# Kernel optimization log

Hardware: AMD Instinct MI355X
Metric: run time of the kernel (lower is better)

Reference implementation:

```python
import jax, jax.numpy as jnp
import numpy as np

N_STEPS = 5
N_ETYPES = 4
N_GRAPHS = 64
HEADS = 2
N, E, D = 50000, 600000, 128
C = 32


def setup_inputs() -> dict:
    key = jax.random.key(0)
    ks = jax.random.split(key, 24)
    s = 0.08  # param scale to keep activations well-conditioned
    return {
        "in_feat1": jax.random.normal(ks[0], (N, D), jnp.float32),
        "in_feat2": jax.random.normal(ks[1], (N, D), jnp.float32),
        "src1": jax.random.randint(ks[2], (E,), 0, N, jnp.int32),
        "dst1": jax.random.randint(ks[3], (E,), 0, N, jnp.int32),
        "etype1": jax.random.randint(ks[4], (E,), 0, N_ETYPES, jnp.int32),
        "gid1": jnp.sort(jax.random.randint(ks[5], (N,), 0, N_GRAPHS, jnp.int32)),
        "src2": jax.random.randint(ks[6], (E,), 0, N, jnp.int32),
        "dst2": jax.random.randint(ks[7], (E,), 0, N, jnp.int32),
        "etype2": jax.random.randint(ks[8], (E,), 0, N_ETYPES, jnp.int32),
        "gid2": jnp.sort(jax.random.randint(ks[9], (N,), 0, N_GRAPHS, jnp.int32)),
        "W_et": jax.random.normal(ks[10], (N_ETYPES, D, D), jnp.float32) * s,
        "b_et": jax.random.normal(ks[11], (N_ETYPES, D), jnp.float32) * s,
        "W_ih": jax.random.normal(ks[12], (3 * D, D), jnp.float32) * s,
        "W_hh": jax.random.normal(ks[13], (3 * D, D), jnp.float32) * s,
        "b_ih": jax.random.normal(ks[14], (3 * D,), jnp.float32) * s,
        "b_hh": jax.random.normal(ks[15], (3 * D,), jnp.float32) * s,
        "W_fc": jax.random.normal(ks[16], (HEADS * D, D), jnp.float32) * s,
        "attn_l": jax.random.normal(ks[17], (HEADS, D), jnp.float32) * s,
        "attn_r": jax.random.normal(ks[18], (HEADS, D), jnp.float32) * s,
        "gat_bias": jax.random.normal(ks[19], (HEADS * D,), jnp.float32) * s,
        "W_cls": jax.random.normal(ks[20], (C, D), jnp.float32) * s,
        "b_cls": jax.random.normal(ks[21], (C,), jnp.float32) * s,
    }


def _ggann(feat, src, dst, etype, gid,
           W_et, b_et, W_ih, W_hh, b_ih, b_hh,
           W_fc, attn_l, attn_r, gat_bias, W_cls, b_cls):
    n = feat.shape[0]
    h = feat  # in_feats == out_feats -> no zero-padding needed
    # ---- GatedGraphConv: n_steps of per-etype message passing + GRU ----
    for _ in range(N_STEPS):
        # per-etype linear on all nodes: [K, N, D]
        t = jnp.einsum('kod,nd->kno', W_et, h) + b_et[:, None, :]
        msg = t[etype, src]                         # [E, D] gather by (etype, src)
        a = jax.ops.segment_sum(msg, dst, num_segments=n)  # [N, D]
        # GRUCell(a, h)
        gi = a @ W_ih.T + b_ih                      # [N, 3D]
        gh = h @ W_hh.T + b_hh
        i_r, i_z, i_n = jnp.split(gi, 3, axis=1)
        h_r, h_z, h_n = jnp.split(gh, 3, axis=1)
        r = jax.nn.sigmoid(i_r + h_r)
        z = jax.nn.sigmoid(i_z + h_z)
        nn_ = jnp.tanh(i_n + r * h_n)
        h = (1.0 - z) * nn_ + z * h
    # F.normalize (L2 over dim=1) then sigmoid
    h = h / jnp.maximum(jnp.linalg.norm(h, axis=1, keepdims=True), 1e-12)
    h = jax.nn.sigmoid(h)
    # ---- GATConv (num_heads=2) ----
    zft = (h @ W_fc.T).reshape(n, HEADS, D)         # [N, H, D]
    el = jnp.sum(zft * attn_l[None], axis=-1)       # [N, H]
    er = jnp.sum(zft * attn_r[None], axis=-1)
    e = jax.nn.leaky_relu(el[src] + er[dst], 0.2)   # [E, H]
    m = jax.ops.segment_max(e, dst, num_segments=n)
    ex = jnp.exp(e - m[dst])
    den = jax.ops.segment_sum(ex, dst, num_segments=n)
    alpha = ex / den[dst]                           # edge softmax per dst, per head
    rst = jax.ops.segment_sum(alpha[:, :, None] * zft[src], dst, num_segments=n)
    rst = rst + gat_bias.reshape(1, HEADS, D)
    h = jax.nn.relu(rst)                            # [N, H, D] (dropout = eval identity)
    # ---- mean_nodes per graph + classify ----
    sums = jax.ops.segment_sum(h, gid, num_segments=N_GRAPHS)      # [B, H, D]
    cnt = jax.ops.segment_sum(jnp.ones((n, 1, 1), h.dtype), gid, num_segments=N_GRAPHS)
    hg = sums / jnp.maximum(cnt, 1.0)
    return hg @ W_cls.T + b_cls                     # [B, H, C]


def reference(in_feat1, in_feat2, src1, dst1, etype1, gid1,
              src2, dst2, etype2, gid2,
              W_et, b_et, W_ih, W_hh, b_ih, b_hh,
              W_fc, attn_l, attn_r, gat_bias, W_cls, b_cls):
    params = (W_et, b_et, W_ih, W_hh, b_ih, b_hh,
              W_fc, attn_l, attn_r, gat_bias, W_cls, b_cls)
    h1 = _ggann(in_feat1, src1, dst1, etype1, gid1, *params)  # [B, H, C]
    h2 = _ggann(in_feat2, src2, dst2, etype2, gid2, *params)
    # F.pairwise_distance(p=2, eps=1e-6) over last dim -> [B, H]
    dist = jnp.linalg.norm(h1 - h2 + 1e-6, axis=-1)
    return jax.nn.softmax(dist, axis=1)             # softmax over the 2 heads
```

## Files before the change

### kernel.cpp

```cpp
#include <hip/hip_runtime.h>
#include <math.h>

#define D 128
#define NG 64
#define NG2 128
#define NSTEPS 5

using short8 = __attribute__((ext_vector_type(8))) short;
using f32x4  = __attribute__((ext_vector_type(4))) float;
using f32x2  = __attribute__((ext_vector_type(2))) float;

__device__ __forceinline__ float sigf(float x) {
  float e = __expf(-fabsf(x));
  float inv = __fdividef(1.f, 1.f + e);
  return x >= 0.f ? inv : e * inv;
}
__device__ __forceinline__ float tanhf_fast(float x) {
  float e = __expf(-2.f * fabsf(x));
  float r = (1.f - e) * __fdividef(1.f, 1.f + e);
  return x >= 0.f ? r : -r;
}
__device__ __forceinline__ float lrelu(float x) { return x > 0.f ? x : 0.2f * x; }
__device__ __forceinline__ short f2bf(float x) {
  unsigned u = __float_as_uint(x);
  u += 0x7fff + ((u >> 16) & 1);
  return (short)(u >> 16);
}
__device__ __forceinline__ unsigned pk2(float x, float y) {
  return ((unsigned)(unsigned short)f2bf(y) << 16) | (unsigned short)f2bf(x);
}
__device__ __forceinline__ float bflo(unsigned v) { return __uint_as_float(v << 16); }
__device__ __forceinline__ float bfhi(unsigned v) { return __uint_as_float(v & 0xffff0000u); }
__device__ __forceinline__ float bf2f(short s) {
  return __uint_as_float(((unsigned)(unsigned short)s) << 16);
}
__device__ __forceinline__ unsigned char f2fp8(float x) {
  int p = __builtin_amdgcn_cvt_pk_fp8_f32(x, x, 0, false);
  return (unsigned char)(p & 0xff);
}

__device__ __forceinline__ void packK128(const float* __restrict__ W,
                                         short* __restrict__ P, int i) {
  int j = i & 7;
  int lane = (i >> 3) & 63;
  int kt = (i >> 9) & 3;
  int nt = i >> 11;
  int c = nt * 16 + (lane & 15);
  int k = kt * 32 + ((lane >> 4) << 3) + j;
  P[i] = f2bf(W[c * 128 + k]);
}
__device__ __forceinline__ void packA512f(const float* __restrict__ W_et,
                                          short* __restrict__ P, int i) {
  int j = i & 7;
  int lane = (i >> 3) & 63;
  int kt = (i >> 9) & 15;
  int nt = i >> 13;
  int c = nt * 16 + (lane & 15);
  int k = kt * 32 + ((lane >> 4) << 3) + j;
  P[i] = f2bf(W_et[(k >> 7) * 16384 + c * 128 + (k & 127)]);
}

__global__ __launch_bounds__(256) void k_setup(const float* __restrict__ W_et,
    const float* __restrict__ W_ih, const float* __restrict__ W_hh,
    const float* __restrict__ W_fc, const float* __restrict__ f1,
    const float* __restrict__ f2, short* __restrict__ WaP, short* __restrict__ WihP,
    short* __restrict__ WhhP, short* __restrict__ WfcP, short* __restrict__ hb,
    unsigned char* __restrict__ hq,
    int* __restrict__ deg, int* __restrict__ gcnt, int N2, int Nd4) {
  const int sA = 65536, sB = 49152, sC = 49152, sD = 32768;
  int sE = N2, sF = NG2;
  long sG = 2L * Nd4;
  long tot = (long)(sA + sB + sC + sD) + sE + sF + sG;
  for (long ii = (long)blockIdx.x * blockDim.x + threadIdx.x; ii < tot;
       ii += (long)gridDim.x * blockDim.x) {
    long r = ii;
    if (r < sA) { packA512f(W_et, WaP, (int)r); continue; }
    r -= sA;
    if (r < sB) { packK128(W_ih, WihP, (int)r); continue; }
    r -= sB;
    if (r < sC) { packK128(W_hh, WhhP, (int)r); continue; }
    r -= sC;
    if (r < sD) { packK128(W_fc, WfcP, (int)r); continue; }
    r -= sD;
    if (r < sE) { deg[r] = 0; continue; }
    r -= sE;
    if (r < sF) { gcnt[r] = 0; continue; }
    r -= sF;
    {
      int i = (int)r;
      float4 v = (i < Nd4) ? ((const float4*)f1)[i] : ((const float4*)f2)[i - Nd4];
      ((uint2*)hb)[i] = make_uint2(pk2(v.x, v.y), pk2(v.z, v.w));
      int q = __builtin_amdgcn_cvt_pk_fp8_f32(v.x, v.y, 0, false);
      q = __builtin_amdgcn_cvt_pk_fp8_f32(v.z, v.w, q, true);
      ((unsigned*)hq)[i] = (unsigned)q;
    }
  }
}

__global__ __launch_bounds__(256) void k_histgid(const int* __restrict__ dst1,
    const int* __restrict__ dst2, const int* __restrict__ gid1,
    const int* __restrict__ gid2, int E, int N, int* __restrict__ deg,
    int* __restrict__ gidc, int* __restrict__ gcnt, int EB, int N2) {
  __shared__ int cnt[NG2];
  if ((int)blockIdx.x < EB) {
    int slice = blockIdx.x & 7;
    int bls = blockIdx.x >> 3;
    int nbs = EB >> 3;
    int W = (N2 + 7) >> 3;
    int lo = slice * W, hi = lo + W;
    for (int e = bls * 256 + threadIdx.x; e < 2 * E; e += nbs * 256) {
      int d = (e < E) ? dst1[e] : dst2[e - E] + N;
      if (d >= lo && d < hi) atomicAdd(&deg[d], 1);
    }
  } else {
    int t = threadIdx.x;
    if (t < NG2) cnt[t] = 0;
    __syncthreads();
    int i = (blockIdx.x - EB) * 256 + t;
    if (i < 2 * N) {
      int g = (i < N) ? gid1[i] : gid2[i - N] + NG;
      gidc[i] = g;
      atomicAdd(&cnt[g], 1);
    }
    __syncthreads();
    if (t < NG2 && cnt[t]) atomicAdd(&gcnt[t], cnt[t]);
  }
}

__global__ __launch_bounds__(256) void k_scan_a(const int* __restrict__ deg, int n,
                                                int* __restrict__ bsum) {
  int base = blockIdx.x * 1024 + threadIdx.x * 4;
  int s = 0;
  if (base + 3 < n) {
    int4 v = *(const int4*)(deg + base);
    s = v.x + v.y + v.z + v.w;
  } else {
    for (int k = 0; k < 4; ++k) if (base + k < n) s += deg[base + k];
  }
  #pragma unroll
  for (int off = 32; off; off >>= 1) s += __shfl_xor(s, off);
  __shared__ int ws[4];
  if ((threadIdx.x & 63) == 0) ws[threadIdx.x >> 6] = s;
  __syncthreads();
  if (threadIdx.x == 0) bsum[blockIdx.x] = ws[0] + ws[1] + ws[2] + ws[3];
}

__global__ __launch_bounds__(1024) void k_scan_b(const int* __restrict__ bsum,
                                                 int* __restrict__ boffs, int nb) {
  int tid = threadIdx.x;
  int v = (tid < nb) ? bsum[tid] : 0;
  int lane = tid & 63, wv = tid >> 6;
  int x = v;
  #pragma unroll
  for (int off = 1; off < 64; off <<= 1) {
    int y = __shfl_up(x, off);
    if (lane >= off) x += y;
  }
  __shared__ int wsum[16];
  if (lane == 63) wsum[wv] = x;
  __syncthreads();
  if (tid < 16) {
    int u = wsum[tid];
    #pragma unroll
    for (int off = 1; off < 16; off <<= 1) {
      int y = __shfl_up(u, off);
      if (tid >= off) u += y;
    }
    wsum[tid] = u;
  }
  __syncthreads();
  int woff = wv ? wsum[wv - 1] : 0;
  if (tid < nb) boffs[tid] = woff + x - v;
}

__global__ __launch_bounds__(256) void k_scan_c(const int* __restrict__ deg,
    const int* __restrict__ boffs, int* __restrict__ row_ofs,
    int* __restrict__ cursor, int n) {
  int base = blockIdx.x * 1024 + threadIdx.x * 4;
  int v[4] = {0, 0, 0, 0};
  if (base + 3 < n) {
    int4 t = *(const int4*)(deg + base);
    v[0] = t.x; v[1] = t.y; v[2] = t.z; v[3] = t.w;
  } else {
    for (int k = 0; k < 4; ++k) if (base + k < n) v[k] = deg[base + k];
  }
  int s = v[0] + v[1] + v[2] + v[3];
  int lane = threadIdx.x & 63, wv = threadIdx.x >> 6;
  int x = s;
  #pragma unroll
  for (int off = 1; off < 64; off <<= 1) {
    int y = __shfl_up(x, off);
    if (lane >= off) x += y;
  }
  __shared__ int wsum[4];
  if (lane == 63) wsum[wv] = x;
  __syncthreads();
  int woff = 0;
  for (int w = 0; w < wv; ++w) woff += wsum[w];
  int run = boffs[blockIdx.x] + woff + x - s;
  #pragma unroll
  for (int k = 0; k < 4; ++k) {
    int i = base + k;
    if (i < n) {
      cursor[i] = run;
      run += v[k];
      row_ofs[i + 1] = run;
    }
  }
  if (blockIdx.x == 0 && threadIdx.x == 0) row_ofs[0] = 0;
}

__global__ __launch_bounds__(256) void k_scatter(const int* __restrict__ src1,
    const int* __restrict__ dst1, const int* __restrict__ ety1,
    const int* __restrict__ src2, const int* __restrict__ dst2,
    const int* __restrict__ ety2, int E, int N, int* __restrict__ cursor,
    int* __restrict__ csr_se, int N2) {
  int slice = blockIdx.x & 7;
  int bls = blockIdx.x >> 3;
  int nbs = gridDim.x >> 3;
  int W = (N2 + 7) >> 3;
  int lo = slice * W, hi = lo + W;
  for (int e = bls * 256 + threadIdx.x; e < 2 * E; e += nbs * 256) {
    int d = (e < E) ? dst1[e] : dst2[e - E] + N;
    if (d < lo || d >= hi) continue;
    int s, et;
    if (e < E) { s = src1[e]; et = ety1[e]; }
    else { s = src2[e - E] + N; et = ety2[e - E]; }
    int p = atomicAdd(&cursor[d], 1);
    csr_se[p] = (s << 10) + et;
  }
}

__global__ __launch_bounds__(1024) void k_step(const unsigned char* __restrict__ hq_old,
    const short* __restrict__ hb_old, unsigned char* __restrict__ hq_new,
    short* __restrict__ hb_new,
    const int* __restrict__ row_ofs, const int* __restrict__ csr_se,
    const short* __restrict__ WaP, const float* __restrict__ b_et,
    const short* __restrict__ Pih, const short* __restrict__ Phh,
    const float* __restrict__ b_ih, const float* __restrict__ b_hh, int M) {
  __shared__ short Stile[16 * 512];
  __shared__ float lcnt[16][4];
  __shared__ short abt[16 * 128];
  __shared__ short hin[16 * 128];
  __shared__ short hbs[16 * 128];
  __shared__ unsigned char hqs[16 * 128];
  int tid = threadIdx.x;
  int lane = tid & 63, wave = tid >> 6;
  int row0 = blockIdx.x * 16;
  int quad = lane >> 4, l15 = lane & 15;

  {
    int li = wave;
    int node = row0 + li;
    f32x2 A0 = {0.f, 0.f}, A1 = {0.f, 0.f}, A2 = {0.f, 0.f}, A3 = {0.f, 0.f};
    int c0 = 0, c1 = 0, c2 = 0, c3 = 0;
    const char* hqb = (const char*)hq_old;
    if (node < M) {
      int beg = row_ofs[node], end = row_ofs[node + 1];
      #define ACC(ET, V) do { \
          f32x2 t_ = __builtin_amdgcn_cvt_pk_f32_fp8((unsigned)(V), false); \
          if (ET == 0)      { A0 += t_; ++c0; } \
          else if (ET == 1) { A1 += t_; ++c1; } \
          else if (ET == 2) { A2 += t_; ++c2; } \
          else              { A3 += t_; ++c3; } } while (0)
      for (int base = beg; base < end; base += 64) {
        int nv = end - base; if (nv > 64) nv = 64;
        int r = (lane < nv) ? csr_se[base + lane] : 0;
        int j = 0;
        for (; j + 16 <= nv; j += 16) {
          int rr[16];
          #pragma unroll
          for (int k = 0; k < 16; ++k) rr[k] = __builtin_amdgcn_readlane(r, j + k);
          unsigned short v[16];
          #pragma unroll
          for (int k = 0; k < 16; ++k)
            v[k] = ((const unsigned short*)(hqb + (rr[k] >> 3)))[lane];
          #pragma unroll
          for (int k = 0; k < 16; ++k) ACC(rr[k] & 3, v[k]);
        }
        for (; j + 8 <= nv; j += 8) {
          int rr[8];
          #pragma unroll
          for (int k = 0; k < 8; ++k) rr[k] = __builtin_amdgcn_readlane(r, j + k);
          unsigned short v[8];
          #pragma unroll
          for (int k = 0; k < 8; ++k)
            v[k] = ((const unsigned short*)(hqb + (rr[k] >> 3)))[lane];
          #pragma unroll
          for (int k = 0; k < 8; ++k) ACC(rr[k] & 3, v[k]);
        }
        for (; j + 4 <= nv; j += 4) {
          int rr[4];
          #pragma unroll
          for (int k = 0; k < 4; ++k) rr[k] = __builtin_amdgcn_readlane(r, j + k);
          unsigned short v[4];
          #pragma unroll
          for (int k = 0; k < 4; ++k)
            v[k] = ((const unsigned short*)(hqb + (rr[k] >> 3)))[lane];
          #pragma unroll
          for (int k = 0; k < 4; ++k) ACC(rr[k] & 3, v[k]);
        }
        for (; j < nv; ++j) {
          int rr = __builtin_amdgcn_readlane(r, j);
          unsigned short v = ((const unsigned short*)(hqb + (rr >> 3)))[lane];
          ACC(rr & 3, v);
        }
      }
      #undef ACC
    }
    int swz = (li & 7) << 4;
    unsigned* ld = (unsigned*)Stile;
    ld[(li * 1024 + ((lane * 4      ) ^ swz)) >> 2] = pk2(A0[0], A0[1]);
    ld[(li * 1024 + ((lane * 4 + 256) ^ swz)) >> 2] = pk2(A1[0], A1[1]);
    ld[(li * 1024 + ((lane * 4 + 512) ^ swz)) >> 2] = pk2(A2[0], A2[1]);
    ld[(li * 1024 + ((lane * 4 + 768) ^ swz)) >> 2] = pk2(A3[0], A3[1]);
    if (lane == 0) {
      lcnt[li][0] = (float)c0; lcnt[li][1] = (float)c1;
      lcnt[li][2] = (float)c2; lcnt[li][3] = (float)c3;
    }
  }
  __syncthreads();

  if (wave < 8) {
    int swz = (l15 & 7) << 4;
    int nt = wave;
    f32x4 acc = {0.f, 0.f, 0.f, 0.f};
    #pragma unroll
    for (int kt = 0; kt < 16; ++kt) {
      int boff = l15 * 1024 + ((kt * 64 + quad * 16) ^ swz);
      short8 a = *(const short8*)((const char*)Stile + boff);
      short8 b = *(const short8*)(WaP + (((size_t)(nt * 16 + kt) * 64) + lane) * 8);
      acc = __builtin_amdgcn_mfma_f32_16x16x32_bf16(a, b, acc, 0, 0, 0);
    }
    int c = nt * 16 + l15;
    float be0 = b_et[c], be1 = b_et[128 + c], be2 = b_et[256 + c], be3 = b_et[384 + c];
    #pragma unroll
    for (int reg = 0; reg < 4; ++reg) {
      int lr = quad * 4 + reg;
      float v = acc[reg] + lcnt[lr][0] * be0 + lcnt[lr][1] * be1
                         + lcnt[lr][2] * be2 + lcnt[lr][3] * be3;
      int bo = (lr * 256 + c * 2) ^ ((lr & 7) << 4);
      *(short*)((char*)abt + bo) = f2bf(v);
    }
  } else if (wave < 12) {
    int t2 = tid - 512;
    int row = t2 >> 4;
    int col8 = t2 & 15;
    int r = row0 + row;
    uint4 v = make_uint4(0, 0, 0, 0);
    if (r < M) v = *(const uint4*)(hb_old + (size_t)r * 128 + col8 * 8);
    int bo = (row * 256 + col8 * 16) ^ ((row & 7) << 4);
    *(uint4*)((char*)hin + bo) = v;
  }
  __syncthreads();

  if (wave < 8) {
    int nt = wave;
    size_t li = ((size_t)lane) * 8;
    f32x4 accr = {0.f,0.f,0.f,0.f}, accz = {0.f,0.f,0.f,0.f};
    f32x4 acci = {0.f,0.f,0.f,0.f}, acch = {0.f,0.f,0.f,0.f};
    #pragma unroll
    for (int kt = 0; kt < 4; ++kt) {
      int ao = (l15 * 256 + (kt * 64 + quad * 16)) ^ ((l15 & 7) << 4);
      short8 fa = *(const short8*)((const char*)abt + ao);
      short8 fh = *(const short8*)((const char*)hin + ao);
      short8 wr = *(const short8*)(Pih + ((size_t)((nt     ) * 4 + kt) * 64) * 8 + li);
      short8 wz = *(const short8*)(Pih + ((size_t)((nt +  8) * 4 + kt) * 64) * 8 + li);
      short8 wn = *(const short8*)(Pih + ((size_t)((nt + 16) * 4 + kt) * 64) * 8 + li);
      short8 ur = *(const short8*)(Phh + ((size_t)((nt     ) * 4 + kt) * 64) * 8 + li);
      short8 uz = *(const short8*)(Phh + ((size_t)((nt +  8) * 4 + kt) * 64) * 8 + li);
      short8 un = *(const short8*)(Phh + ((size_t)((nt + 16) * 4 + kt) * 64) * 8 + li);
      accr = __builtin_amdgcn_mfma_f32_16x16x32_bf16(fa, wr, accr, 0, 0, 0);
      accr = __builtin_amdgcn_mfma_f32_16x16x32_bf16(fh, ur, accr, 0, 0, 0);
      accz = __builtin_amdgcn_mfma_f32_16x16x32_bf16(fa, wz, accz, 0, 0, 0);
      accz = __builtin_amdgcn_mfma_f32_16x16x32_bf16(fh, uz, accz, 0, 0, 0);
      acci = __builtin_amdgcn_mfma_f32_16x16x32_bf16(fa, wn, acci, 0, 0, 0);
      acch = __builtin_amdgcn_mfma_f32_16x16x32_bf16(fh, un, acch, 0, 0, 0);
    }
    int c = nt * 16 + l15;
    float bir = b_ih[c],      bhr = b_hh[c];
    float biz = b_ih[c+128],  bhz = b_hh[c+128];
    float bin_= b_ih[c+256],  bhn = b_hh[c+256];
    #pragma unroll
    for (int reg = 0; reg < 4; ++reg) {
      int lr = quad * 4 + reg;
      float rgate = sigf(accr[reg] + bir + bhr);
      float zg = sigf(accz[reg] + biz + bhz);
      float ng = tanhf_fast(acci[reg] + bin_ + rgate * (acch[reg] + bhn));
      int ho = (lr * 256 + c * 2) ^ ((lr & 7) << 4);
      float hold = bf2f(*(const short*)((const char*)hin + ho));
      float hn2 = (1.f - zg) * ng + zg * hold;
      hbs[lr * 128 + c] = f2bf(hn2);
      hqs[lr * 128 + c] = f2fp8(hn2);
    }
  }
  __syncthreads();

  if (tid < 256) {
    int off16 = tid * 8;
    int grow = off16 >> 7;
    if (row0 + grow < M)
      *(uint4*)(hb_new + (size_t)row0 * 128 + off16) = *(const uint4*)&hbs[off16];
  } else if (tid < 384) {
    int offb = (tid - 256) * 16;
    int grow = offb >> 7;
    if (row0 + grow < M)
      *(uint4*)(hq_new + (size_t)row0 * 128 + offb) = *(const uint4*)&hqs[offb];
  }
}

__global__ __launch_bounds__(256) void k_fc_eler(const short* __restrict__ Ab,
    const short* __restrict__ Bp, const float* __restrict__ attn_l,
    const float* __restrict__ attn_r, unsigned char* __restrict__ zq,
    float* __restrict__ el, float* __restrict__ er, int M) {
  int tid = threadIdx.x;
  int lane = tid & 63, wave = tid >> 6;
  int row0 = blockIdx.x * 128 + wave * 32;
  int quad = lane >> 4, l15 = lane & 15;
  short8 af[2][4];
  #pragma unroll
  for (int rt = 0; rt < 2; ++rt) {
    int ar = row0 + rt * 16 + l15; if (ar >= M) ar = M - 1;
    #pragma unroll
    for (int kt = 0; kt < 4; ++kt)
      af[rt][kt] = *(const short8*)(Ab + (size_t)ar * 128 + kt * 32 + quad * 8);
  }
  #pragma unroll
  for (int rt = 0; rt < 2; ++rt) {
    float ss = 0.f;
    #pragma unroll
    for (int kt = 0; kt < 4; ++kt)
      #pragma unroll
      for (int j = 0; j < 8; ++j) {
        float x = bf2f(af[rt][kt][j]);
        ss += x * x;
      }
    ss += __shfl_xor(ss, 16);
    ss += __shfl_xor(ss, 32);
    float inv = 1.f / fmaxf(sqrtf(ss), 1e-12f);
    #pragma unroll
    for (int kt = 0; kt < 4; ++kt)
      #pragma unroll
      for (int j = 0; j < 8; ++j)
        af[rt][kt][j] = f2bf(sigf(bf2f(af[rt][kt][j]) * inv));
  }
  float elp[2][2][4] = {};
  float erp[2][2][4] = {};
  for (int nt = 0; nt < 16; ++nt) {
    f32x4 a0 = {0.f,0.f,0.f,0.f}, a1 = {0.f,0.f,0.f,0.f};
    #pragma unroll
    for (int kt = 0; kt < 4; ++kt) {
      short8 b = *(const short8*)(Bp + (((size_t)(nt * 4 + kt) * 64) + lane) * 8);
      a0 = __builtin_amdgcn_mfma_f32_16x16x32_bf16(af[0][kt], b, a0, 0, 0, 0);
      a1 = __builtin_amdgcn_mfma_f32_16x16x32_bf16(af[1][kt], b, a1, 0, 0, 0);
    }
    int head = nt >> 3;
    int colh = (nt & 7) * 16 + l15;
    float alv = attn_l[head * 128 + colh];
    float arv = attn_r[head * 128 + colh];
    int c = nt * 16 + l15;
    #pragma unroll
    for (int rt = 0; rt < 2; ++rt) {
      f32x4 acc = rt ? a1 : a0;
      #pragma unroll
      for (int reg = 0; reg < 4; ++reg) {
        int r = row0 + rt * 16 + quad * 4 + reg;
        if (r < M) zq[(size_t)r * 256 + c] = f2fp8(acc[reg]);
        elp[rt][head][reg] += acc[reg] * alv;
        erp[rt][head][reg] += acc[reg] * arv;
      }
    }
  }
  #pragma unroll
  for (int off = 1; off < 16; off <<= 1) {
    #pragma unroll
    for (int rt = 0; rt < 2; ++rt)
      #pragma unroll
      for (int h = 0; h < 2; ++h)
        #pragma unroll
        for (int reg = 0; reg < 4; ++reg) {
          elp[rt][h][reg] += __shfl_xor(elp[rt][h][reg], off);
          erp[rt][h][reg] += __shfl_xor(erp[rt][h][reg], off);
        }
  }
  if (l15 == 0) {
    #pragma unroll
    for (int rt = 0; rt < 2; ++rt)
      #pragma unroll
      for (int h = 0; h < 2; ++h)
        #pragma unroll
        for (int reg = 0; reg < 4; ++reg) {
          int r = row0 + rt * 16 + quad * 4 + reg;
          if (r < M) {
            el[r * 2 + h] = elp[rt][h][reg];
            er[r * 2 + h] = erp[rt][h][reg];
          }
        }
  }
}

__global__ __launch_bounds__(256) void k_gat(const unsigned char* __restrict__ zq,
    const float* __restrict__ el, const float* __restrict__ er,
    const int* __restrict__ row_ofs, const int* __restrict__ csr_se,
    const float* __restrict__ gat_bias, short* __restrict__ outb,
    float* __restrict__ sums, int N) {
  if (blockIdx.x < NG2) sums[blockIdx.x * 256 + threadIdx.x] = 0.f;
  int node = blockIdx.x * 4 + (threadIdx.x >> 6);
  int lane = threadIdx.x & 63;
  if (node >= N) return;
  int beg = row_ofs[node], end = row_ofs[node + 1];
  float2 ern = ((const float2*)er)[node];
  float l0 = 0.f, l1 = 0.f;
  float4 acc = {0.f, 0.f, 0.f, 0.f};
  int head = lane >> 5;
  const char* elb = (const char*)el;
  const char* zqb = (const char*)zq;
  for (int base = beg; base < end; base += 64) {
    int nv = end - base; if (nv > 64) nv = 64;
    int se = (lane < nv) ? csr_se[base + lane] : 0;
    float p0 = 0.f, p1 = 0.f;
    if (lane < nv) {
      float2 els = *(const float2*)(elb + (se >> 7));
      p0 = expf(lrelu(els.x + ern.x));
      p1 = expf(lrelu(els.y + ern.y));
    }
    float t0 = p0, t1 = p1;
    #pragma unroll
    for (int off = 32; off; off >>= 1) { t0 += __shfl_xor(t0, off); t1 += __shfl_xor(t1, off); }
    l0 += t0; l1 += t1;
    int w01 = (int)pk2(p0, p1);
    int j = 0;
    for (; j + 8 <= nv; j += 8) {
      int bb[8]; unsigned ww[8];
      #pragma unroll
      for (int k = 0; k < 8; ++k) {
        bb[k] = __builtin_amdgcn_readlane(se, j + k) >> 2;
        ww[k] = (unsigned)__builtin_amdgcn_readlane(w01, j + k);
      }
      unsigned zz[8];
      #pragma unroll
      for (int k = 0; k < 8; ++k)
        zz[k] = ((const unsigned*)(zqb + bb[k]))[lane];
      #pragma unroll
      for (int k = 0; k < 8; ++k) {
        float f = head ? bfhi(ww[k]) : bflo(ww[k]);
        f32x2 lo = __builtin_amdgcn_cvt_pk_f32_fp8(zz[k], false);
        f32x2 hi = __builtin_amdgcn_cvt_pk_f32_fp8(zz[k], true);
        acc.x += f * lo[0]; acc.y += f * lo[1];
        acc.z += f * hi[0]; acc.w += f * hi[1];
      }
    }
    for (; j + 4 <= nv; j += 4) {
      int bb[4]; unsigned ww[4];
      #pragma unroll
      for (int k = 0; k < 4; ++k) {
        bb[k] = __builtin_amdgcn_readlane(se, j + k) >> 2;
        ww[k] = (unsigned)__builtin_amdgcn_readlane(w01, j + k);
      }
      unsigned zz[4];
      #pragma unroll
      for (int k = 0; k < 4; ++k)
        zz[k] = ((const unsigned*)(zqb + bb[k]))[lane];
      #pragma unroll
      for (int k = 0; k < 4; ++k) {
        float f = head ? bfhi(ww[k]) : bflo(ww[k]);
        f32x2 lo = __builtin_amdgcn_cvt_pk_f32_fp8(zz[k], false);
        f32x2 hi = __builtin_amdgcn_cvt_pk_f32_fp8(zz[k], true);
        acc.x += f * lo[0]; acc.y += f * lo[1];
        acc.z += f * hi[0]; acc.w += f * hi[1];
      }
    }
    for (; j < nv; ++j) {
      int bj = __builtin_amdgcn_readlane(se, j) >> 2;
      unsigned wj = (unsigned)__builtin_amdgcn_readlane(w01, j);
      float w = head ? bfhi(wj) : bflo(wj);
      unsigned zv = ((const unsigned*)(zqb + bj))[lane];
      f32x2 lo = __builtin_amdgcn_cvt_pk_f32_fp8(zv, false);
      f32x2 hi = __builtin_amdgcn_cvt_pk_f32_fp8(zv, true);
      acc.x += w * lo[0]; acc.y += w * lo[1];
      acc.z += w * hi[0]; acc.w += w * hi[1];
    }
  }
  float inv0 = (l0 > 0.f) ? 1.f / l0 : 0.f;
  float inv1 = (l1 > 0.f) ? 1.f / l1 : 0.f;
  float inv = head ? inv1 : inv0;
  float4 b = ((const float4*)gat_bias)[lane];
  float ox = fmaxf(acc.x * inv + b.x, 0.f);
  float oy = fmaxf(acc.y * inv + b.y, 0.f);
  float oz = fmaxf(acc.z * inv + b.z, 0.f);
  float ow = fmaxf(acc.w * inv + b.w, 0.f);
  ((uint2*)(outb + (size_t)node * 256))[lane] = make_uint2(pk2(ox, oy), pk2(oz, ow));
}

__global__ __launch_bounds__(256) void k_segred(const short* __restrict__ hgatb,
    const int* __restrict__ gidc, float* __restrict__ sums, int NT2) {
  int node0 = blockIdx.x * 128;
  int col = threadIdx.x;
  int end = node0 + 128; if (end > NT2) end = NT2;
  if (node0 >= NT2) return;
  float acc = 0.f;
  int gcur = gidc[node0];
  for (int n = node0; n < end; ++n) {
    int g = gidc[n];
    if (g != gcur) {
      atomicAdd(&sums[gcur * 256 + col], acc);
      acc = 0.f; gcur = g;
    }
    acc += bf2f(hgatb[(size_t)n * 256 + col]);
  }
  atomicAdd(&sums[gcur * 256 + col], acc);
}

__global__ __launch_bounds__(64) void k_classify(const float* __restrict__ sums,
    const int* __restrict__ gcnt, const float* __restrict__ W_cls,
    const float* __restrict__ b_cls, float* __restrict__ logits) {
  int g = blockIdx.x, tid = threadIdx.x;
  int hh = tid >> 5, c = tid & 31;
  float invc = 1.f / fmaxf((float)gcnt[g], 1.f);
  float acc = 0.f;
  for (int d = 0; d < D; ++d)
    acc += (sums[g * 256 + hh * D + d] * invc) * W_cls[c * D + d];
  logits[g * 64 + hh * 32 + c] = acc + b_cls[c];
}

__global__ __launch_bounds__(64) void k_final(const float* __restrict__ logits,
    float* __restrict__ out) {
  int g = threadIdx.x;
  if (g >= NG) return;
  float d[2];
  #pragma unroll
  for (int hh = 0; hh < 2; ++hh) {
    float s = 0.f;
    for (int c = 0; c < 32; ++c) {
      float df = logits[g * 64 + hh * 32 + c] - logits[(g + NG) * 64 + hh * 32 + c] + 1e-6f;
      s += df * df;
    }
    d[hh] = sqrtf(s);
  }
  float mx = fmaxf(d[0], d[1]);
  float e0 = expf(d[0] - mx), e1 = expf(d[1] - mx);
  float den = e0 + e1;
  out[g * 2] = e0 / den;
  out[g * 2 + 1] = e1 / den;
}

extern "C" void kernel_launch(void* const* d_in, const int* in_sizes, int n_in,
                              void* d_out, int out_size, void* d_ws, size_t ws_size,
                              hipStream_t stream) {
  const float* in_feat1 = (const float*)d_in[0];
  const float* in_feat2 = (const float*)d_in[1];
  const int* src1 = (const int*)d_in[2];
  const int* dst1 = (const int*)d_in[3];
  const int* ety1 = (const int*)d_in[4];
  const int* gid1 = (const int*)d_in[5];
  const int* src2 = (const int*)d_in[6];
  const int* dst2 = (const int*)d_in[7];
  const int* ety2 = (const int*)d_in[8];
  const int* gid2 = (const int*)d_in[9];
  const float* W_et = (const float*)d_in[10];
  const float* b_et = (const float*)d_in[11];
  const float* W_ih = (const float*)d_in[12];
  const float* W_hh = (const float*)d_in[13];
  const float* b_ih = (const float*)d_in[14];
  const float* b_hh = (const float*)d_in[15];
  const float* W_fc = (const float*)d_in[16];
  const float* attn_l = (const float*)d_in[17];
  const float* attn_r = (const float*)d_in[18];
  const float* gat_bias = (const float*)d_in[19];
  const float* W_cls = (const float*)d_in[20];
  const float* b_cls = (const float*)d_in[21];
  float* out = (float*)d_out;

  int N = in_sizes[0] / D;
  int E = in_sizes[2];
  int N2 = 2 * N, E2 = 2 * E;

  char* p = (char*)d_ws;
  auto alloc = [&](size_t bytes) -> void* {
    char* r = p;
    p += (bytes + 255) & ~(size_t)255;
    return (void*)r;
  };
  short* WaP  = (short*)alloc((size_t)512 * 128 * 2);
  short* WihP = (short*)alloc((size_t)384 * 128 * 2);
  short* WhhP = (short*)alloc((size_t)384 * 128 * 2);
  short* WfcP = (short*)alloc((size_t)256 * 128 * 2);
  short* hb0 = (short*)alloc((size_t)N2 * D * 2);
  short* hb1 = (short*)alloc((size_t)N2 * D * 2);
  unsigned char* hq0 = (unsigned char*)alloc((size_t)N2 * D);
  unsigned char* hq1 = (unsigned char*)alloc((size_t)N2 * D);
  short* hgatb = (short*)alloc((size_t)N2 * 256 * 2);
  unsigned char* zq = (unsigned char*)alloc((size_t)N2 * 256);
  float* el  = (float*)alloc((size_t)N2 * 2 * 4);
  float* er  = (float*)alloc((size_t)N2 * 2 * 4);
  float* sums= (float*)alloc((size_t)NG2 * 256 * 4);
  float* logits = (float*)alloc((size_t)NG2 * 64 * 4);
  int* deg     = (int*)alloc((size_t)N2 * 4);
  int* row_ofs = (int*)alloc(((size_t)N2 + 1) * 4);
  int* cursor  = (int*)alloc((size_t)N2 * 4);
  int* gidc    = (int*)alloc((size_t)N2 * 4);
  int* gcnt    = (int*)alloc((size_t)NG2 * 4);
  int* bsum    = (int*)alloc((size_t)1024 * 4);
  int* boffs   = (int*)alloc((size_t)1024 * 4);
  int* csr_se  = (int*)alloc((size_t)E2 * 4);
  if ((size_t)(p - (char*)d_ws) > ws_size) return;

  k_setup<<<dim3(2048), dim3(256), 0, stream>>>(W_et, W_ih, W_hh, W_fc,
      in_feat1, in_feat2, WaP, WihP, WhhP, WfcP, hb0, hq0, deg, gcnt, N2, N * D / 4);

  int EB = 4800;
  int GB = (N2 + 255) / 256;
  int nb = (N2 + 1023) / 1024;
  k_histgid<<<dim3(EB + GB), dim3(256), 0, stream>>>(dst1, dst2, gid1, gid2,
                                                     E, N, deg, gidc, gcnt, EB, N2);
  k_scan_a<<<dim3(nb), dim3(256), 0, stream>>>(deg, N2, bsum);
  k_scan_b<<<dim3(1), dim3(1024), 0, stream>>>(bsum, boffs, nb);
  k_scan_c<<<dim3(nb), dim3(256), 0, stream>>>(deg, boffs, row_ofs, cursor, N2);
  k_scatter<<<dim3(4800), dim3(256), 0, stream>>>(src1, dst1, ety1, src2, dst2, ety2,
                                                  E, N, cursor, csr_se, N2);

  int gb16 = (N2 + 15) / 16;
  int gb128 = (N2 + 127) / 128;
  int nb4 = (N2 + 3) / 4;

  short* hbp[2] = {hb0, hb1};
  unsigned char* hqp[2] = {hq0, hq1};
  for (int s = 0; s < NSTEPS; ++s) {
    k_step<<<dim3(gb16), dim3(1024), 0, stream>>>(
        hqp[s & 1], hbp[s & 1], hqp[(s + 1) & 1], hbp[(s + 1) & 1],
        row_ofs, csr_se, WaP, b_et, WihP, WhhP, b_ih, b_hh, N2);
  }
  short* hbf = hbp[NSTEPS & 1];
  k_fc_eler<<<dim3(gb128), dim3(256), 0, stream>>>(hbf, WfcP, attn_l, attn_r, zq, el, er, N2);
  k_gat<<<dim3(nb4), dim3(256), 0, stream>>>(zq, el, er, row_ofs, csr_se,
                                             gat_bias, hgatb, sums, N2);
  k_segred<<<dim3((N2 + 127) / 128), dim3(256), 0, stream>>>(hgatb, gidc, sums, N2);
  k_classify<<<dim3(NG2), dim3(64), 0, stream>>>(sums, gcnt, W_cls, b_cls, logits);
  k_final<<<dim3(1), dim3(64), 0, stream>>>(logits, out);
}
```

Before: 1.004 ms.

## Process 32 rows per k_step block and use packed FMAs in GAT gather

k_step now covers 32 nodes per 1024-thread block: each wave gathers two nodes, and all 16 waves take part in both MFMA phases as two 16-row tiles. The old-h load is folded into the gather loop instead of using a separate wave group. This halves the weight-fragment traffic per node and removes the phases where half the waves sat idle. The trade-offs are a larger LDS footprint, half as many blocks, and a longer serial gather per wave. Separately, k_gat accumulates into f32x2 vectors so the compiler can emit packed FMAs.

```diff
diff --git a/kernel.cpp b/kernel.cpp
--- a/kernel.cpp
+++ b/kernel.cpp
@@ -238,19 +238,20 @@
     const short* __restrict__ WaP, const float* __restrict__ b_et,
     const short* __restrict__ Pih, const short* __restrict__ Phh,
     const float* __restrict__ b_ih, const float* __restrict__ b_hh, int M) {
-  __shared__ short Stile[16 * 512];
-  __shared__ float lcnt[16][4];
-  __shared__ short abt[16 * 128];
-  __shared__ short hin[16 * 128];
-  __shared__ short hbs[16 * 128];
-  __shared__ unsigned char hqs[16 * 128];
+  __shared__ short Stile[32 * 512];
+  __shared__ float lcnt[32][4];
+  __shared__ short abt[32 * 128];
+  __shared__ short hin[32 * 128];
+  __shared__ short hbs[32 * 128];
+  __shared__ unsigned char hqs[32 * 128];
   int tid = threadIdx.x;
   int lane = tid & 63, wave = tid >> 6;
-  int row0 = blockIdx.x * 16;
+  int row0 = blockIdx.x * 32;
   int quad = lane >> 4, l15 = lane & 15;
 
-  {
-    int li = wave;
+  #pragma unroll
+  for (int i = 0; i < 2; ++i) {
+    int li = wave * 2 + i;
     int node = row0 + li;
     f32x2 A0 = {0.f, 0.f}, A1 = {0.f, 0.f}, A2 = {0.f, 0.f}, A3 = {0.f, 0.f};
     int c0 = 0, c1 = 0, c2 = 0, c3 = 0;
@@ -318,16 +319,20 @@
       lcnt[li][0] = (float)c0; lcnt[li][1] = (float)c1;
       lcnt[li][2] = (float)c2; lcnt[li][3] = (float)c3;
     }
+    unsigned hv = (node < M) ? ((const unsigned*)(hb_old + (size_t)node * 128))[lane] : 0u;
+    *(unsigned*)((char*)hin + (li * 256 + ((lane * 4) ^ swz))) = hv;
   }
   __syncthreads();
 
-  if (wave < 8) {
+  {
+    int tile = wave >> 3;
+    int nt = wave & 7;
+    int srow = tile * 16 + l15;
     int swz = (l15 & 7) << 4;
-    int nt = wave;
     f32x4 acc = {0.f, 0.f, 0.f, 0.f};
     #pragma unroll
     for (int kt = 0; kt < 16; ++kt) {
-      int boff = l15 * 1024 + ((kt * 64 + quad * 16) ^ swz);
+      int boff = srow * 1024 + ((kt * 64 + quad * 16) ^ swz);
       short8 a = *(const short8*)((const char*)Stile + boff);
       short8 b = *(const short8*)(WaP + (((size_t)(nt * 16 + kt) * 64) + lane) * 8);
       acc = __builtin_amdgcn_mfma_f32_16x16x32_bf16(a, b, acc, 0, 0, 0);
@@ -336,32 +341,26 @@
     float be0 = b_et[c], be1 = b_et[128 + c], be2 = b_et[256 + c], be3 = b_et[384 + c];
     #pragma unroll
     for (int reg = 0; reg < 4; ++reg) {
-      int lr = quad * 4 + reg;
+      int lr = tile * 16 + quad * 4 + reg;
       float v = acc[reg] + lcnt[lr][0] * be0 + lcnt[lr][1] * be1
                          + lcnt[lr][2] * be2 + lcnt[lr][3] * be3;
-      int bo = (lr * 256 + c * 2) ^ ((lr & 7) << 4);
+      int bo = (lr * 256 + ((c * 2) ^ ((lr & 7) << 4)));
       *(short*)((char*)abt + bo) = f2bf(v);
     }
-  } else if (wave < 12) {
-    int t2 = tid - 512;
-    int row = t2 >> 4;
-    int col8 = t2 & 15;
-    int r = row0 + row;
-    uint4 v = make_uint4(0, 0, 0, 0);
-    if (r < M) v = *(const uint4*)(hb_old + (size_t)r * 128 + col8 * 8);
-    int bo = (row * 256 + col8 * 16) ^ ((row & 7) << 4);
-    *(uint4*)((char*)hin + bo) = v;
   }
   __syncthreads();
 
-  if (wave < 8) {
-    int nt = wave;
+  {
+    int tile = wave >> 3;
+    int nt = wave & 7;
     size_t li = ((size_t)lane) * 8;
+    int srow = tile * 16 + l15;
+    int swz = (l15 & 7) << 4;
     f32x4 accr = {0.f,0.f,0.f,0.f}, accz = {0.f,0.f,0.f,0.f};
     f32x4 acci = {0.f,0.f,0.f,0.f}, acch = {0.f,0.f,0.f,0.f};
     #pragma unroll
     for (int kt = 0; kt < 4; ++kt) {
-      int ao = (l15 * 256 + (kt * 64 + quad * 16)) ^ ((l15 & 7) << 4);
+      int ao = srow * 256 + ((kt * 64 + quad * 16) ^ swz);
       short8 fa = *(const short8*)((const char*)abt + ao);
       short8 fh = *(const short8*)((const char*)hin + ao);
       short8 wr = *(const short8*)(Pih + ((size_t)((nt     ) * 4 + kt) * 64) * 8 + li);
@@ -383,11 +382,11 @@
     float bin_= b_ih[c+256],  bhn = b_hh[c+256];
     #pragma unroll
     for (int reg = 0; reg < 4; ++reg) {
-      int lr = quad * 4 + reg;
+      int lr = tile * 16 + quad * 4 + reg;
       float rgate = sigf(accr[reg] + bir + bhr);
       float zg = sigf(accz[reg] + biz + bhz);
       float ng = tanhf_fast(acci[reg] + bin_ + rgate * (acch[reg] + bhn));
-      int ho = (lr * 256 + c * 2) ^ ((lr & 7) << 4);
+      int ho = lr * 256 + (((c * 2) ^ ((lr & 7) << 4)));
       float hold = bf2f(*(const short*)((const char*)hin + ho));
       float hn2 = (1.f - zg) * ng + zg * hold;
       hbs[lr * 128 + c] = f2bf(hn2);
@@ -396,13 +395,13 @@
   }
   __syncthreads();
 
-  if (tid < 256) {
+  if (tid < 512) {
     int off16 = tid * 8;
     int grow = off16 >> 7;
     if (row0 + grow < M)
       *(uint4*)(hb_new + (size_t)row0 * 128 + off16) = *(const uint4*)&hbs[off16];
-  } else if (tid < 384) {
-    int offb = (tid - 256) * 16;
+  } else if (tid < 768) {
+    int offb = (tid - 512) * 16;
     int grow = offb >> 7;
     if (row0 + grow < M)
       *(uint4*)(hq_new + (size_t)row0 * 128 + offb) = *(const uint4*)&hqs[offb];
@@ -511,7 +510,7 @@
   int beg = row_ofs[node], end = row_ofs[node + 1];
   float2 ern = ((const float2*)er)[node];
   float l0 = 0.f, l1 = 0.f;
-  float4 acc = {0.f, 0.f, 0.f, 0.f};
+  f32x2 a01 = {0.f, 0.f}, a23 = {0.f, 0.f};
   int head = lane >> 5;
   const char* elb = (const char*)el;
   const char* zqb = (const char*)zq;
@@ -544,10 +543,11 @@
       #pragma unroll
       for (int k = 0; k < 8; ++k) {
         float f = head ? bfhi(ww[k]) : bflo(ww[k]);
+        f32x2 fv = {f, f};
         f32x2 lo = __builtin_amdgcn_cvt_pk_f32_fp8(zz[k], false);
         f32x2 hi = __builtin_amdgcn_cvt_pk_f32_fp8(zz[k], true);
-        acc.x += f * lo[0]; acc.y += f * lo[1];
-        acc.z += f * hi[0]; acc.w += f * hi[1];
+        a01 = lo * fv + a01;
+        a23 = hi * fv + a23;
       }
     }
     for (; j + 4 <= nv; j += 4) {
@@ -564,31 +564,33 @@
       #pragma unroll
       for (int k = 0; k < 4; ++k) {
         float f = head ? bfhi(ww[k]) : bflo(ww[k]);
+        f32x2 fv = {f, f};
         f32x2 lo = __builtin_amdgcn_cvt_pk_f32_fp8(zz[k], false);
         f32x2 hi = __builtin_amdgcn_cvt_pk_f32_fp8(zz[k], true);
-        acc.x += f * lo[0]; acc.y += f * lo[1];
-        acc.z += f * hi[0]; acc.w += f * hi[1];
+        a01 = lo * fv + a01;
+        a23 = hi * fv + a23;
       }
     }
     for (; j < nv; ++j) {
       int bj = __builtin_amdgcn_readlane(se, j) >> 2;
       unsigned wj = (unsigned)__builtin_amdgcn_readlane(w01, j);
       float w = head ? bfhi(wj) : bflo(wj);
+      f32x2 fv = {w, w};
       unsigned zv = ((const unsigned*)(zqb + bj))[lane];
       f32x2 lo = __builtin_amdgcn_cvt_pk_f32_fp8(zv, false);
       f32x2 hi = __builtin_amdgcn_cvt_pk_f32_fp8(zv, true);
-      acc.x += w * lo[0]; acc.y += w * lo[1];
-      acc.z += w * hi[0]; acc.w += w * hi[1];
+      a01 = lo * fv + a01;
+      a23 = hi * fv + a23;
     }
   }
   float inv0 = (l0 > 0.f) ? 1.f / l0 : 0.f;
   float inv1 = (l1 > 0.f) ? 1.f / l1 : 0.f;
   float inv = head ? inv1 : inv0;
   float4 b = ((const float4*)gat_bias)[lane];
-  float ox = fmaxf(acc.x * inv + b.x, 0.f);
-  float oy = fmaxf(acc.y * inv + b.y, 0.f);
-  float oz = fmaxf(acc.z * inv + b.z, 0.f);
-  float ow = fmaxf(acc.w * inv + b.w, 0.f);
+  float ox = fmaxf(a01[0] * inv + b.x, 0.f);
+  float oy = fmaxf(a01[1] * inv + b.y, 0.f);
+  float oz = fmaxf(a23[0] * inv + b.z, 0.f);
+  float ow = fmaxf(a23[1] * inv + b.w, 0.f);
   ((uint2*)(outb + (size_t)node * 256))[lane] = make_uint2(pk2(ox, oy), pk2(oz, ow));
 }
 
@@ -719,14 +721,14 @@
   k_scatter<<<dim3(4800), dim3(256), 0, stream>>>(src1, dst1, ety1, src2, dst2, ety2,
                                                   E, N, cursor, csr_se, N2);
 
-  int gb16 = (N2 + 15) / 16;
+  int gb32 = (N2 + 31) / 32;
   int gb128 = (N2 + 127) / 128;
   int nb4 = (N2 + 3) / 4;
 
   short* hbp[2] = {hb0, hb1};
   unsigned char* hqp[2] = {hq0, hq1};
   for (int s = 0; s < NSTEPS; ++s) {
-    k_step<<<dim3(gb16), dim3(1024), 0, stream>>>(
+    k_step<<<dim3(gb32), dim3(1024), 0, stream>>>(
         hqp[s & 1], hbp[s & 1], hqp[(s + 1) & 1], hbp[(s + 1) & 1],
         row_ofs, csr_se, WaP, b_et, WihP, WhhP, b_ih, b_hh, N2);
   }
```

Result: slower. 1.186 ms (+18.2%).
